# Kernel optimization log

Measured on AMD Instinct MI355X. Metric: run time of the kernel, lower is better.

Reference implementation:

```python
import jax, jax.numpy as jnp
import numpy as np

EPS = 1e-06
NUM_HEADS = 16


def _rms_norm(x, g, eps=EPS):
    # normalize over the last (full model) dim, as WanRMSNorm(dim)
    var = jnp.mean(jnp.square(x), axis=-1, keepdims=True)
    return x * jax.lax.rsqrt(var + eps) * g


def _apply_rope(q, k, freqs):
    # q, k: [b, s, n, d]; freqs: [s, d//2] angles. Interleaved (complex) pairs
    b, s, n, d = q.shape
    cos = jnp.cos(freqs)[None, :, None, :]  # [1, s, 1, d//2]
    sin = jnp.sin(freqs)[None, :, None, :]

    def rot(t):
        tr = t.reshape(b, s, n, d // 2, 2)
        t0, t1 = tr[..., 0], tr[..., 1]
        o0 = t0 * cos - t1 * sin
        o1 = t0 * sin + t1 * cos
        return jnp.stack([o0, o1], axis=-1).reshape(b, s, n, d)

    return rot(q), rot(k)


def setup_inputs() -> dict:
    key = jax.random.key(0)
    ks = jax.random.split(key, 8)
    b, s, dim = 2, 2048, 2048
    hd = dim // NUM_HEADS
    x = jax.random.normal(ks[0], (b, s, dim), dtype=jnp.float32)
    seq_lens = jax.random.randint(ks[1], (b,), s // 2, s + 1, dtype=jnp.int32)
    grid_sizes = jax.random.randint(ks[2], (b, 3), 1, 16).astype(jnp.int64)
    freqs = jax.random.uniform(ks[3], (s, hd // 2), dtype=jnp.float32) * 6.283
    sc = 1.0 / np.sqrt(dim)
    Wq = jax.random.normal(ks[4], (dim, dim), dtype=jnp.float32) * sc
    Wk = jax.random.normal(ks[5], (dim, dim), dtype=jnp.float32) * sc
    Wv = jax.random.normal(ks[6], (dim, dim), dtype=jnp.float32) * sc
    Wo = jax.random.normal(ks[7], (dim, dim), dtype=jnp.float32) * sc
    bo = jnp.zeros((dim,), dtype=jnp.float32)
    gq = jnp.ones((dim,), dtype=jnp.float32)
    gk = jnp.ones((dim,), dtype=jnp.float32)
    return {"x": x, "seq_lens": seq_lens, "grid_sizes": grid_sizes, "freqs": freqs,
            "Wq": Wq, "Wk": Wk, "Wv": Wv, "Wo": Wo, "bo": bo, "gq": gq, "gk": gk}


def reference(x, seq_lens, grid_sizes, freqs, Wq, Wk, Wv, Wo, bo, gq, gk):
    b, s, dim = x.shape
    n = NUM_HEADS
    d = dim // n
    scale = d ** (-0.5)

    # QKV projections (Linear: x @ W.T), with RMSNorm over full dim on q/k
    q = _rms_norm(x @ Wq.T, gq).reshape(b, s, n, d)
    k = _rms_norm(x @ Wk.T, gk).reshape(b, s, n, d)
    v = (x @ Wv.T).reshape(b, s, n, d)

    q, k = _apply_rope(q, k, freqs)

    # varlen attention: keys beyond seq_lens[b] are masked out
    scores = jnp.einsum("bqnd,bknd->bnqk", q, k) * scale
    key_valid = jnp.arange(s)[None, None, None, :] < seq_lens[:, None, None, None]
    scores = jnp.where(key_valid, scores, jnp.float32(-1e9))
    probs = jax.nn.softmax(scores, axis=-1)
    attn = jnp.einsum("bnqk,bknd->bqnd", probs, v).reshape(b, s, dim)

    return attn @ Wo.T + bo
```

## Files before the change

### kernel.cpp

```cpp
#include <hip/hip_runtime.h>
#include <hip/hip_bf16.h>
#include <math.h>

#define BATCH 2
#define SEQ   2048
#define DIM   2048
#define NH    16
#define HD    128
#define NROWS (BATCH * SEQ)
#define EPS_RMS 1e-6f

typedef unsigned short ushort_t;
typedef unsigned int   uint_t;
typedef __bf16    bf16x8 __attribute__((ext_vector_type(8)));
typedef _Float16  f16x8  __attribute__((ext_vector_type(8)));
typedef float     f32x4  __attribute__((ext_vector_type(4)));

__device__ inline ushort_t f2bf(float f) {
    uint_t u = __builtin_bit_cast(uint_t, f);
    uint_t r = u + 0x7FFFu + ((u >> 16) & 1u);
    return (ushort_t)(r >> 16);
}
__device__ inline ushort_t f2h(float f) {
    return __builtin_bit_cast(ushort_t, (_Float16)f);
}

__global__ __launch_bounds__(256) void cvt_all_kernel(
    const float* __restrict__ x,  const float* __restrict__ wq,
    const float* __restrict__ wk, const float* __restrict__ wv,
    const float* __restrict__ wo,
    ushort_t* __restrict__ xh,  ushort_t* __restrict__ wqh,
    ushort_t* __restrict__ wkh, ushort_t* __restrict__ wvh,
    ushort_t* __restrict__ woh)
{
    const int blk = blockIdx.x;
    const float* src; ushort_t* dst; size_t base;
    if (blk < 4096) { src = x; dst = xh; base = (size_t)blk * 2048; }
    else {
        const int r = blk - 4096;
        const int wsel = r >> 11;
        base = (size_t)(r & 2047) * 2048;
        if      (wsel == 0) { src = wq; dst = wqh; }
        else if (wsel == 1) { src = wk; dst = wkh; }
        else if (wsel == 2) { src = wv; dst = wvh; }
        else                { src = wo; dst = woh; }
    }
    const size_t i = base + ((size_t)threadIdx.x << 3);
    float v[8];
    *(float4*)&v[0] = *(const float4*)&src[i];
    *(float4*)&v[4] = *(const float4*)&src[i + 4];
    uint_t pk[4];
#pragma unroll
    for (int j = 0; j < 4; ++j)
        pk[j] = (uint_t)f2h(v[2 * j]) | ((uint_t)f2h(v[2 * j + 1]) << 16);
    *(uint4*)&dst[i] = make_uint4(pk[0], pk[1], pk[2], pk[3]);
}

template<int MODE>
__global__ __launch_bounds__(256, 2) void gemm_f16_kernel(
    const ushort_t* __restrict__ Ah, const ushort_t* __restrict__ Bh,
    const float* __restrict__ bias,
    float* __restrict__ C, ushort_t* __restrict__ Ct,
    const int M, const int N, const int K)
{
    __shared__ __align__(16) ushort_t sA[4096], sB[4096];
    const int tid  = threadIdx.x;
    const int w    = tid >> 6;
    const int lane = tid & 63;
    const int m0 = blockIdx.y * 128;
    const int n0 = blockIdx.x * 128;

    const int scol = (lane & 3) << 3;
    const int wr = w >> 1, wc = w & 1;
    const int fr = lane & 15, quad = lane >> 4;

    f32x4 acc[4][4];
#pragma unroll
    for (int mi = 0; mi < 4; ++mi)
#pragma unroll
        for (int ni = 0; ni < 4; ++ni)
            acc[mi][ni] = (f32x4){0.f, 0.f, 0.f, 0.f};

    for (int k0 = 0; k0 < K; k0 += 32) {
        __syncthreads();
#pragma unroll
        for (int it = 0; it < 2; ++it) {
            const int row  = (w << 5) + (it << 4) + (lane >> 2);
            const int loff = (w << 10) + (it << 9);
            const size_t ga = (size_t)(m0 + row) * K + k0 + scol;
            const size_t gb = (size_t)(n0 + row) * K + k0 + scol;
            __builtin_amdgcn_global_load_lds(
                (const __attribute__((address_space(1))) uint_t*)(const void*)(Ah + ga),
                (__attribute__((address_space(3))) uint_t*)(void*)&sA[loff], 16, 0, 0);
            __builtin_amdgcn_global_load_lds(
                (const __attribute__((address_space(1))) uint_t*)(const void*)(Bh + gb),
                (__attribute__((address_space(3))) uint_t*)(void*)&sB[loff], 16, 0, 0);
        }
        __syncthreads();

        f16x8 bfr[4];
#pragma unroll
        for (int ni = 0; ni < 4; ++ni) {
            const int row = (wc << 6) + (ni << 4) + fr;
            bfr[ni] = *(const f16x8*)&sB[(row << 5) + (quad << 3)];
        }
#pragma unroll
        for (int mi = 0; mi < 4; ++mi) {
            const int row = (wr << 6) + (mi << 4) + fr;
            const f16x8 ah = *(const f16x8*)&sA[(row << 5) + (quad << 3)];
#pragma unroll
            for (int ni = 0; ni < 4; ++ni)
                acc[mi][ni] = __builtin_amdgcn_mfma_f32_16x16x32_f16(ah, bfr[ni], acc[mi][ni], 0, 0, 0);
        }
    }

#pragma unroll
    for (int mi = 0; mi < 4; ++mi)
#pragma unroll
        for (int ni = 0; ni < 4; ++ni) {
            const int col = n0 + (wc << 6) + (ni << 4) + fr;
            if (MODE == 0) {
                const float bv = bias ? bias[col] : 0.f;
#pragma unroll
                for (int r = 0; r < 4; ++r) {
                    const int rowg = m0 + (wr << 6) + (mi << 4) + (quad << 2) + r;
                    C[(size_t)rowg * N + col] = acc[mi][ni][r] + bv;
                }
            } else {
                const int rowg = m0 + (wr << 6) + (mi << 4) + (quad << 2);
                const int bb = rowg >> 11, tok = rowg & (SEQ - 1);
                const int hh = col >> 7, d = col & (HD - 1);
                uint2 pk;
                pk.x = (uint_t)f2bf(acc[mi][ni][0]) | ((uint_t)f2bf(acc[mi][ni][1]) << 16);
                pk.y = (uint_t)f2bf(acc[mi][ni][2]) | ((uint_t)f2bf(acc[mi][ni][3]) << 16);
                *(uint2*)&Ct[((size_t)(bb * NH + hh) * HD + d) * SEQ + tok] = pk;
            }
        }
}

__global__ __launch_bounds__(256, 3) void qkv_gemm_kernel(
    const ushort_t* __restrict__ Ah, const ushort_t* __restrict__ Bq,
    const ushort_t* __restrict__ Bk, const ushort_t* __restrict__ Bv,
    float* __restrict__ Qb, float* __restrict__ Kb, ushort_t* __restrict__ Vt)
{
    __shared__ __align__(16) ushort_t sA[4096], sB[4096];
    const int tid  = threadIdx.x;
    const int w    = tid >> 6;
    const int lane = tid & 63;

    const int bid = blockIdx.x;
    const int nid = (bid & 7) * 192 + (bid >> 3);
    const int n_blk = nid >> 5;
    const int m_blk = nid & 31;
    const int wsel  = n_blk >> 4;
    const int m0 = m_blk * 128;
    const int n0 = (n_blk & 15) * 128;
    const ushort_t* __restrict__ Bh = (wsel == 0) ? Bq : (wsel == 1) ? Bk : Bv;

    const int scol = (lane & 3) << 3;
    const int wr = w >> 1, wc = w & 1;
    const int fr = lane & 15, quad = lane >> 4;

    f32x4 acc[4][4];
#pragma unroll
    for (int mi = 0; mi < 4; ++mi)
#pragma unroll
        for (int ni = 0; ni < 4; ++ni)
            acc[mi][ni] = (f32x4){0.f, 0.f, 0.f, 0.f};

    for (int k0 = 0; k0 < DIM; k0 += 32) {
        __syncthreads();
#pragma unroll
        for (int it = 0; it < 2; ++it) {
            const int row  = (w << 5) + (it << 4) + (lane >> 2);
            const int loff = (w << 10) + (it << 9);
            const size_t ga = (size_t)(m0 + row) * DIM + k0 + scol;
            const size_t gb = (size_t)(n0 + row) * DIM + k0 + scol;
            __builtin_amdgcn_global_load_lds(
                (const __attribute__((address_space(1))) uint_t*)(const void*)(Ah + ga),
                (__attribute__((address_space(3))) uint_t*)(void*)&sA[loff], 16, 0, 0);
            __builtin_amdgcn_global_load_lds(
                (const __attribute__((address_space(1))) uint_t*)(const void*)(Bh + gb),
                (__attribute__((address_space(3))) uint_t*)(void*)&sB[loff], 16, 0, 0);
        }
        __syncthreads();

        f16x8 bfr[4];
#pragma unroll
        for (int ni = 0; ni < 4; ++ni) {
            const int row = (wc << 6) + (ni << 4) + fr;
            bfr[ni] = *(const f16x8*)&sB[(row << 5) + (quad << 3)];
        }
#pragma unroll
        for (int mi = 0; mi < 4; ++mi) {
            const int row = (wr << 6) + (mi << 4) + fr;
            const f16x8 ah = *(const f16x8*)&sA[(row << 5) + (quad << 3)];
#pragma unroll
            for (int ni = 0; ni < 4; ++ni)
                acc[mi][ni] = __builtin_amdgcn_mfma_f32_16x16x32_f16(ah, bfr[ni], acc[mi][ni], 0, 0, 0);
        }
    }

    if (wsel < 2) {
        float* __restrict__ C = (wsel == 0) ? Qb : Kb;
#pragma unroll
        for (int mi = 0; mi < 4; ++mi)
#pragma unroll
            for (int ni = 0; ni < 4; ++ni) {
                const int col = n0 + (wc << 6) + (ni << 4) + fr;
#pragma unroll
                for (int r = 0; r < 4; ++r) {
                    const int rowg = m0 + (wr << 6) + (mi << 4) + (quad << 2) + r;
                    C[(size_t)rowg * DIM + col] = acc[mi][ni][r];
                }
            }
    } else {
#pragma unroll
        for (int mi = 0; mi < 4; ++mi)
#pragma unroll
            for (int ni = 0; ni < 4; ++ni) {
                const int col = n0 + (wc << 6) + (ni << 4) + fr;
                const int rowg = m0 + (wr << 6) + (mi << 4) + (quad << 2);
                const int bb = rowg >> 11, tok = rowg & (SEQ - 1);
                const int hh = col >> 7, d = col & (HD - 1);
                uint2 pk;
                pk.x = (uint_t)f2bf(acc[mi][ni][0]) | ((uint_t)f2bf(acc[mi][ni][1]) << 16);
                pk.y = (uint_t)f2bf(acc[mi][ni][2]) | ((uint_t)f2bf(acc[mi][ni][3]) << 16);
                *(uint2*)&Vt[((size_t)(bb * NH + hh) * HD + d) * SEQ + tok] = pk;
            }
    }
}

#define BM 64
#define BN 64
#define BK 16

__global__ __launch_bounds__(256) void gemm_nt_kernel(
    const float* __restrict__ A, const float* __restrict__ W,
    const float* __restrict__ bias, float* __restrict__ C,
    const int M, const int N, const int K)
{
    __shared__ float As[BK][BM + 4];
    __shared__ float Bs[BK][BN + 4];
    const int tid = threadIdx.x;
    const int tx = tid & 15;
    const int ty = tid >> 4;
    const int m0 = blockIdx.y * BM;
    const int n0 = blockIdx.x * BN;
    const int ldr = tid >> 2;
    const int ldc = (tid & 3) << 2;

    float acc[4][4] = {};

    for (int k0 = 0; k0 < K; k0 += BK) {
        __syncthreads();
        const float4 av = *(const float4*)&A[(size_t)(m0 + ldr) * K + (k0 + ldc)];
        const float4 wv = *(const float4*)&W[(size_t)(n0 + ldr) * K + (k0 + ldc)];
        As[ldc + 0][ldr] = av.x; As[ldc + 1][ldr] = av.y;
        As[ldc + 2][ldr] = av.z; As[ldc + 3][ldr] = av.w;
        Bs[ldc + 0][ldr] = wv.x; Bs[ldc + 1][ldr] = wv.y;
        Bs[ldc + 2][ldr] = wv.z; Bs[ldc + 3][ldr] = wv.w;
        __syncthreads();
#pragma unroll
        for (int k = 0; k < BK; ++k) {
            const float4 a4 = *(const float4*)&As[k][ty << 2];
            const float4 b4 = *(const float4*)&Bs[k][tx << 2];
            const float aa[4] = {a4.x, a4.y, a4.z, a4.w};
            const float bb[4] = {b4.x, b4.y, b4.z, b4.w};
#pragma unroll
            for (int i = 0; i < 4; ++i)
#pragma unroll
                for (int j = 0; j < 4; ++j)
                    acc[i][j] = fmaf(aa[i], bb[j], acc[i][j]);
        }
    }

#pragma unroll
    for (int i = 0; i < 4; ++i) {
        const int row = m0 + (ty << 2) + i;
        const int col = n0 + (tx << 2);
        float4 ov;
        ov.x = acc[i][0]; ov.y = acc[i][1]; ov.z = acc[i][2]; ov.w = acc[i][3];
        if (bias != nullptr) {
            ov.x += bias[col + 0]; ov.y += bias[col + 1];
            ov.z += bias[col + 2]; ov.w += bias[col + 3];
        }
        *(float4*)&C[(size_t)row * N + col] = ov;
    }
}

__global__ __launch_bounds__(256) void rmsnorm_rope_qk_kernel(
    const float* __restrict__ Qb, const float* __restrict__ gq,
    ushort_t* __restrict__ qbh,
    const float* __restrict__ Kb, const float* __restrict__ gk,
    ushort_t* __restrict__ kbh,
    const float* __restrict__ freqs)
{
    const int r = blockIdx.x;
    const int s = r & (SEQ - 1);
    const int tid = threadIdx.x;
    const int base = tid << 3;
    const bool isQ = (blockIdx.y == 0);
    const float* T = isQ ? Qb : Kb;
    const float* g = isQ ? gq : gk;
    ushort_t* out  = isQ ? qbh : kbh;
    const float posc = isQ ? 0.088388347648318447f : 1.0f;

    float v[8];
    *(float4*)&v[0] = *(const float4*)&T[(size_t)r * DIM + base];
    *(float4*)&v[4] = *(const float4*)&T[(size_t)r * DIM + base + 4];

    float ss = 0.f;
#pragma unroll
    for (int i = 0; i < 8; ++i) ss += v[i] * v[i];
#pragma unroll
    for (int off = 32; off > 0; off >>= 1) ss += __shfl_down(ss, off);

    __shared__ float wsum[4];
    __shared__ float inv_sh;
    if ((tid & 63) == 0) wsum[tid >> 6] = ss;
    __syncthreads();
    if (tid == 0)
        inv_sh = rsqrtf((wsum[0] + wsum[1] + wsum[2] + wsum[3]) * (1.0f / DIM) + EPS_RMS);
    __syncthreads();
    const float inv = inv_sh * posc;

    float gg[8];
    *(float4*)&gg[0] = *(const float4*)&g[base];
    *(float4*)&gg[4] = *(const float4*)&g[base + 4];
#pragma unroll
    for (int i = 0; i < 8; ++i) v[i] *= inv * gg[i];

    const int p0 = (base & (HD - 1)) >> 1;
#pragma unroll
    for (int pp = 0; pp < 4; ++pp) {
        float sn, cs;
        __sincosf(freqs[(size_t)s * (HD / 2) + p0 + pp], &sn, &cs);
        const float t0 = v[2 * pp], t1 = v[2 * pp + 1];
        v[2 * pp]     = t0 * cs - t1 * sn;
        v[2 * pp + 1] = t0 * sn + t1 * cs;
    }

    uint_t pk[4];
#pragma unroll
    for (int j = 0; j < 4; ++j)
        pk[j] = (uint_t)f2bf(v[2 * j]) | ((uint_t)f2bf(v[2 * j + 1]) << 16);
    *(uint4*)&out[(size_t)r * DIM + base] = make_uint4(pk[0], pk[1], pk[2], pk[3]);
}

__global__ __launch_bounds__(256) void rmsnorm_rope_kernel(
    float* __restrict__ T, const float* __restrict__ g,
    const float* __restrict__ freqs)
{
    const int r = blockIdx.x;
    const int s = r & (SEQ - 1);
    const int tid = threadIdx.x;
    const int base = tid << 3;

    float v[8];
    *(float4*)&v[0] = *(const float4*)&T[(size_t)r * DIM + base];
    *(float4*)&v[4] = *(const float4*)&T[(size_t)r * DIM + base + 4];

    float ss = 0.f;
#pragma unroll
    for (int i = 0; i < 8; ++i) ss += v[i] * v[i];
#pragma unroll
    for (int off = 32; off > 0; off >>= 1) ss += __shfl_down(ss, off);

    __shared__ float wsum[4];
    __shared__ float inv_sh;
    if ((tid & 63) == 0) wsum[tid >> 6] = ss;
    __syncthreads();
    if (tid == 0)
        inv_sh = rsqrtf((wsum[0] + wsum[1] + wsum[2] + wsum[3]) * (1.0f / DIM) + EPS_RMS);
    __syncthreads();
    const float inv = inv_sh;

    float gg[8];
    *(float4*)&gg[0] = *(const float4*)&g[base];
    *(float4*)&gg[4] = *(const float4*)&g[base + 4];
#pragma unroll
    for (int i = 0; i < 8; ++i) v[i] *= inv * gg[i];

    const int p0 = (base & (HD - 1)) >> 1;
#pragma unroll
    for (int pp = 0; pp < 4; ++pp) {
        float sn, cs;
        __sincosf(freqs[(size_t)s * (HD / 2) + p0 + pp], &sn, &cs);
        const float t0 = v[2 * pp], t1 = v[2 * pp + 1];
        v[2 * pp]     = t0 * cs - t1 * sn;
        v[2 * pp + 1] = t0 * sn + t1 * cs;
    }

    *(float4*)&T[(size_t)r * DIM + base]     = *(float4*)&v[0];
    *(float4*)&T[(size_t)r * DIM + base + 4] = *(float4*)&v[4];
}

#define AQ 128
#define AK 64
#define KSTR 136
#define VSTR 72
#define RESCALE_THR 8.0f

__global__ __launch_bounds__(256, 2) void attn_mfma_kernel(
    const ushort_t* __restrict__ QH, const ushort_t* __restrict__ KH,
    const ushort_t* __restrict__ VtG, const int* __restrict__ seq_lens,
    ushort_t* __restrict__ Oh)
{
    __shared__ __align__(16) ushort_t sK[AK * KSTR];
    __shared__ __align__(16) ushort_t sVt[HD * VSTR];
    __shared__ __align__(16) ushort_t sP[AQ * VSTR];

    const int tid  = threadIdx.x;
    const int w    = tid >> 6;
    const int lane = tid & 63;
    const int fr   = lane & 15;
    const int quad = lane >> 4;

    const int bid = blockIdx.x;
    const int sw  = (bid & 7) * 64 + (bid >> 3);
    const int q0  = (sw & 15) * AQ;
    const int hb  = sw >> 4;
    const int h   = hb & 15;
    const int b   = hb >> 4;
    const int len = seq_lens[b];

    bf16x8 qfrag[2][4];
#pragma unroll
    for (int qt = 0; qt < 2; ++qt)
#pragma unroll
        for (int h4 = 0; h4 < 4; ++h4) {
            const size_t qrow = (size_t)(b * SEQ + q0 + (w << 5) + (qt << 4) + fr);
            qfrag[qt][h4] = *(const bf16x8*)&QH[qrow * DIM + h * HD + (h4 << 5) + (quad << 3)];
        }

    f32x4 Oacc[2][8];
#pragma unroll
    for (int qt = 0; qt < 2; ++qt)
#pragma unroll
        for (int dt = 0; dt < 8; ++dt)
            Oacc[qt][dt] = (f32x4){0.f, 0.f, 0.f, 0.f};
    float mrow[2] = {-1.0e30f, -1.0e30f};
    float lrow[2] = {0.f, 0.f};

    const int ntiles = (len + AK - 1) / AK;
    for (int t = 0; t < ntiles; ++t) {
        const int k0 = t * AK;
        const bool masked = (k0 + AK > len);
        __syncthreads();
        for (int i = tid; i < AK * 16; i += 256) {
            const int key = i >> 4, c8 = (i & 15) << 3;
            const uint4 kv = *(const uint4*)&KH[(size_t)(b * SEQ + k0 + key) * DIM + h * HD + c8];
            *(uint4*)&sK[key * KSTR + c8] = kv;
        }
        for (int i = tid; i < HD * 8; i += 256) {
            const int d = i >> 3, kc = (i & 7) << 3;
            const uint4 vv = *(const uint4*)&VtG[((size_t)(b * NH + h) * HD + d) * SEQ + k0 + kc];
            *(uint4*)&sVt[d * VSTR + kc] = vv;
        }
        __syncthreads();

        f32x4 S[4][2];
        __builtin_amdgcn_s_setprio(1);
#pragma unroll
        for (int kt = 0; kt < 4; ++kt) {
            bf16x8 kf[4];
#pragma unroll
            for (int h4 = 0; h4 < 4; ++h4)
                kf[h4] = *(const bf16x8*)&sK[((kt << 4) + fr) * KSTR + (h4 << 5) + (quad << 3)];
#pragma unroll
            for (int qt = 0; qt < 2; ++qt) {
                f32x4 a = (f32x4){0.f, 0.f, 0.f, 0.f};
#pragma unroll
                for (int h4 = 0; h4 < 4; ++h4)
                    a = __builtin_amdgcn_mfma_f32_16x16x32_bf16(kf[h4], qfrag[qt][h4], a, 0, 0, 0);
                S[kt][qt] = a;
            }
        }
        __builtin_amdgcn_s_setprio(0);

#pragma unroll
        for (int qt = 0; qt < 2; ++qt) {
            float tm = -1.0e30f;
            if (masked) {
#pragma unroll
                for (int kt = 0; kt < 4; ++kt)
#pragma unroll
                    for (int r = 0; r < 4; ++r) {
                        const int key = k0 + (kt << 4) + (quad << 2) + r;
                        float s = (key < len) ? S[kt][qt][r] : -1.0e30f;
                        S[kt][qt][r] = s;
                        tm = fmaxf(tm, s);
                    }
            } else {
#pragma unroll
                for (int kt = 0; kt < 4; ++kt)
#pragma unroll
                    for (int r = 0; r < 4; ++r)
                        tm = fmaxf(tm, S[kt][qt][r]);
            }
            tm = fmaxf(tm, __shfl_xor(tm, 16));
            tm = fmaxf(tm, __shfl_xor(tm, 32));

            float mnew;
            if (__all(tm - mrow[qt] <= RESCALE_THR)) {
                mnew = mrow[qt];
            } else {
                mnew = fmaxf(mrow[qt], tm);
                const float alpha = __expf(mrow[qt] - mnew);
                mrow[qt] = mnew;
                lrow[qt] *= alpha;
#pragma unroll
                for (int r = 0; r < 4; ++r) {
                    const float ar = __shfl(alpha, (quad << 2) + r);
#pragma unroll
                    for (int dt = 0; dt < 8; ++dt)
                        Oacc[qt][dt][r] *= ar;
                }
            }

            float rsum = 0.f;
#pragma unroll
            for (int kt = 0; kt < 4; ++kt) {
                float p[4];
#pragma unroll
                for (int r = 0; r < 4; ++r) {
                    p[r] = __expf(S[kt][qt][r] - mnew);
                    rsum += p[r];
                }
                uint2 pk;
                pk.x = (uint_t)f2bf(p[0]) | ((uint_t)f2bf(p[1]) << 16);
                pk.y = (uint_t)f2bf(p[2]) | ((uint_t)f2bf(p[3]) << 16);
                *(uint2*)&sP[((w << 5) + (qt << 4) + fr) * VSTR + (kt << 4) + (quad << 2)] = pk;
            }
            rsum += __shfl_xor(rsum, 16);
            rsum += __shfl_xor(rsum, 32);
            lrow[qt] += rsum;
        }

        __builtin_amdgcn_s_setprio(1);
#pragma unroll
        for (int ks = 0; ks < 2; ++ks) {
            bf16x8 pf[2];
#pragma unroll
            for (int qt = 0; qt < 2; ++qt)
                pf[qt] = *(const bf16x8*)&sP[((w << 5) + (qt << 4) + fr) * VSTR + (ks << 5) + (quad << 3)];
#pragma unroll
            for (int dt = 0; dt < 8; ++dt) {
                const bf16x8 vf = *(const bf16x8*)&sVt[((dt << 4) + fr) * VSTR + (ks << 5) + (quad << 3)];
#pragma unroll
                for (int qt = 0; qt < 2; ++qt)
                    Oacc[qt][dt] = __builtin_amdgcn_mfma_f32_16x16x32_bf16(pf[qt], vf, Oacc[qt][dt], 0, 0, 0);
            }
        }
        __builtin_amdgcn_s_setprio(0);
    }

#pragma unroll
    for (int qt = 0; qt < 2; ++qt) {
        float linv[4];
#pragma unroll
        for (int r = 0; r < 4; ++r)
            linv[r] = 1.0f / __shfl(lrow[qt], (quad << 2) + r);
#pragma unroll
        for (int dt = 0; dt < 8; ++dt)
#pragma unroll
            for (int r = 0; r < 4; ++r) {
                const int qrow = q0 + (w << 5) + (qt << 4) + (quad << 2) + r;
                Oh[(size_t)(b * SEQ + qrow) * DIM + h * HD + (dt << 4) + fr] =
                    f2h(Oacc[qt][dt][r] * linv[r]);
            }
    }
}

#define BQ  64
#define BKT 64

__global__ __launch_bounds__(256) void attn_kernel(
    const float* __restrict__ Q, const float* __restrict__ K,
    const float* __restrict__ V, const int* __restrict__ seq_lens,
    float* __restrict__ O)
{
    const int qt = blockIdx.x;
    const int h  = blockIdx.y;
    const int b  = blockIdx.z;
    const int len = seq_lens[b];
    const int q0 = qt * BQ;
    const float scale = 0.088388347648318447f;

    __shared__ float Qst[HD][BQ + 4];
    __shared__ float Kst[HD][BKT + 4];
    __shared__ float Vs[BKT][HD + 4];
    __shared__ float Sc[BQ][BKT + 1];
    __shared__ float mrow[BQ], lrow[BQ], alpha_s[BQ];

    const int tid = threadIdx.x;
    const int si0 = (tid >> 4) << 2;
    const int sj0 = (tid & 15) << 2;
    const int pi0 = (tid >> 4) << 2;
    const int pc0 = (tid & 15) << 3;

    for (int i = tid; i < BQ * HD / 4; i += 256) {
        const int e = i << 2;
        const int row = e >> 7;
        const int c0 = e & (HD - 1);
        const float4 qv = *(const float4*)&Q[(size_t)(b * SEQ + q0 + row) * DIM + h * HD + c0];
        Qst[c0 + 0][row] = qv.x; Qst[c0 + 1][row] = qv.y;
        Qst[c0 + 2][row] = qv.z; Qst[c0 + 3][row] = qv.w;
    }
    if (tid < BQ) { mrow[tid] = -3.0e38f; lrow[tid] = 0.f; }

    float o[4][8] = {};
    __syncthreads();

    const int ntiles = (len + BKT - 1) / BKT;
    for (int t = 0; t < ntiles; ++t) {
        const int k0 = t * BKT;
        __syncthreads();
        for (int i = tid; i < BKT * HD / 4; i += 256) {
            const int e = i << 2;
            const int row = e >> 7;
            const int c0 = e & (HD - 1);
            const int kg = k0 + row;
            float4 kv = make_float4(0.f, 0.f, 0.f, 0.f);
            float4 vv = make_float4(0.f, 0.f, 0.f, 0.f);
            if (kg < len) {
                kv = *(const float4*)&K[(size_t)(b * SEQ + kg) * DIM + h * HD + c0];
                vv = *(const float4*)&V[(size_t)(b * SEQ + kg) * DIM + h * HD + c0];
            }
            Kst[c0 + 0][row] = kv.x; Kst[c0 + 1][row] = kv.y;
            Kst[c0 + 2][row] = kv.z; Kst[c0 + 3][row] = kv.w;
            *(float4*)&Vs[row][c0] = vv;
        }
        __syncthreads();

        float acc[4][4] = {};
#pragma unroll 8
        for (int kk = 0; kk < HD; ++kk) {
            const float4 q4 = *(const float4*)&Qst[kk][si0];
            const float4 k4 = *(const float4*)&Kst[kk][sj0];
            const float qa[4] = {q4.x, q4.y, q4.z, q4.w};
            const float ka[4] = {k4.x, k4.y, k4.z, k4.w};
#pragma unroll
            for (int i = 0; i < 4; ++i)
#pragma unroll
                for (int j = 0; j < 4; ++j)
                    acc[i][j] = fmaf(qa[i], ka[j], acc[i][j]);
        }
#pragma unroll
        for (int i = 0; i < 4; ++i)
#pragma unroll
            for (int j = 0; j < 4; ++j) {
                const int jg = k0 + sj0 + j;
                Sc[si0 + i][sj0 + j] = (jg < len) ? acc[i][j] * scale : -1.0e9f;
            }
        __syncthreads();

        if (tid < BQ) {
            const int i = tid;
            const float m_old = mrow[i];
            float mx = m_old;
            for (int j = 0; j < BKT; ++j) mx = fmaxf(mx, Sc[i][j]);
            const float al = __expf(m_old - mx);
            float sum = 0.f;
            for (int j = 0; j < BKT; ++j) {
                const float p = __expf(Sc[i][j] - mx);
                Sc[i][j] = p;
                sum += p;
            }
            mrow[i] = mx;
            lrow[i] = lrow[i] * al + sum;
            alpha_s[i] = al;
        }
        __syncthreads();

#pragma unroll
        for (int i = 0; i < 4; ++i) {
            const float al = alpha_s[pi0 + i];
#pragma unroll
            for (int c = 0; c < 8; ++c) o[i][c] *= al;
        }
        for (int j = 0; j < BKT; ++j) {
            float p[4];
#pragma unroll
            for (int i = 0; i < 4; ++i) p[i] = Sc[pi0 + i][j];
            const float4 v0 = *(const float4*)&Vs[j][pc0];
            const float4 v1 = *(const float4*)&Vs[j][pc0 + 4];
            const float va[8] = {v0.x, v0.y, v0.z, v0.w, v1.x, v1.y, v1.z, v1.w};
#pragma unroll
            for (int i = 0; i < 4; ++i)
#pragma unroll
                for (int c = 0; c < 8; ++c)
                    o[i][c] = fmaf(p[i], va[c], o[i][c]);
        }
    }

#pragma unroll
    for (int i = 0; i < 4; ++i) {
        const float invl = 1.0f / lrow[pi0 + i];
        float4 w0, w1;
        w0.x = o[i][0] * invl; w0.y = o[i][1] * invl;
        w0.z = o[i][2] * invl; w0.w = o[i][3] * invl;
        w1.x = o[i][4] * invl; w1.y = o[i][5] * invl;
        w1.z = o[i][6] * invl; w1.w = o[i][7] * invl;
        float* op = &O[(size_t)(b * SEQ + q0 + pi0 + i) * DIM + h * HD + pc0];
        *(float4*)&op[0] = w0;
        *(float4*)&op[4] = w1;
    }
}

extern "C" void kernel_launch(void* const* d_in, const int* in_sizes, int n_in,
                              void* d_out, int out_size, void* d_ws, size_t ws_size,
                              hipStream_t stream)
{
    const float* x        = (const float*)d_in[0];
    const int*   seq_lens = (const int*)d_in[1];
    const float* freqs    = (const float*)d_in[3];
    const float* Wq       = (const float*)d_in[4];
    const float* Wk       = (const float*)d_in[5];
    const float* Wv       = (const float*)d_in[6];
    const float* Wo       = (const float*)d_in[7];
    const float* bo       = (const float*)d_in[8];
    const float* gq       = (const float*)d_in[9];
    const float* gk       = (const float*)d_in[10];
    float* out = (float*)d_out;

    const size_t mat = (size_t)NROWS * DIM;
    const size_t wsz = (size_t)DIM * DIM;

    float*    Qb   = (float*)d_ws;
    float*    Kb   = Qb + mat;
    ushort_t* xh   = (ushort_t*)(Kb + mat);
    ushort_t* wqh  = xh + mat;
    ushort_t* wkh  = wqh + wsz;
    ushort_t* wvh  = wkh + wsz;
    ushort_t* woh  = wvh + wsz;
    ushort_t* qbh  = woh + wsz;
    ushort_t* kbh  = qbh + mat;
    ushort_t* vtg  = kbh + mat;
    ushort_t* abh  = vtg + mat;

    const size_t need = 2 * mat * sizeof(float)
                      + (mat + 4 * wsz + 4 * mat) * sizeof(ushort_t);

    if (ws_size >= need) {
        cvt_all_kernel<<<12288, 256, 0, stream>>>(
            x, Wq, Wk, Wv, Wo, xh, wqh, wkh, wvh, woh);

        qkv_gemm_kernel<<<1536, 256, 0, stream>>>(xh, wqh, wkh, wvh, Qb, Kb, vtg);

        rmsnorm_rope_qk_kernel<<<dim3(NROWS, 2), 256, 0, stream>>>(
            Qb, gq, qbh, Kb, gk, kbh, freqs);

        attn_mfma_kernel<<<512, 256, 0, stream>>>(qbh, kbh, vtg, seq_lens, abh);

        const dim3 gg(DIM / 128, NROWS / 128);
        gemm_f16_kernel<0><<<gg, 256, 0, stream>>>(abh, woh, bo, out, nullptr, NROWS, DIM, DIM);
    } else {
        float* Vb = Kb + mat;
        float* Ab = Vb + mat;
        const dim3 gemm_grid(DIM / BN, NROWS / BM);
        gemm_nt_kernel<<<gemm_grid, 256, 0, stream>>>(x, Wq, nullptr, Qb, NROWS, DIM, DIM);
        gemm_nt_kernel<<<gemm_grid, 256, 0, stream>>>(x, Wk, nullptr, Kb, NROWS, DIM, DIM);
        gemm_nt_kernel<<<gemm_grid, 256, 0, stream>>>(x, Wv, nullptr, Vb, NROWS, DIM, DIM);
        rmsnorm_rope_kernel<<<NROWS, 256, 0, stream>>>(Qb, gq, freqs);
        rmsnorm_rope_kernel<<<NROWS, 256, 0, stream>>>(Kb, gk, freqs);
        attn_kernel<<<dim3(SEQ / BQ, NH, BATCH), 256, 0, stream>>>(Qb, Kb, Vb, seq_lens, Ab);
        gemm_nt_kernel<<<gemm_grid, 256, 0, stream>>>(Ab, Wo, bo, out, NROWS, DIM, DIM);
    }
}
```

Baseline: 511.1 us.

## Raise occupancy, remap output GEMM blocks across XCDs, batch attention tile loads

Raises launch_bounds min blocks from 2 to 3 for the f16 GEMM and attention kernels so more waves can be resident per CU. Switches the output projection GEMM to a 1D grid whose block index is swizzled so each of the 8 XCDs gets a contiguous chunk of tiles, column-major over M, to improve L2 reuse of weight tiles. Unrolls the attention K/V tile copy into four independent global loads per thread issued before the LDS stores, to increase memory-level parallelism. The tighter register budget may cause spills in the MFMA-heavy kernels.

```diff
diff --git a/kernel.cpp b/kernel.cpp
--- a/kernel.cpp
+++ b/kernel.cpp
@@ -57,7 +57,7 @@
 }
 
 template<int MODE>
-__global__ __launch_bounds__(256, 2) void gemm_f16_kernel(
+__global__ __launch_bounds__(256, 3) void gemm_f16_kernel(
     const ushort_t* __restrict__ Ah, const ushort_t* __restrict__ Bh,
     const float* __restrict__ bias,
     float* __restrict__ C, ushort_t* __restrict__ Ct,
@@ -67,8 +67,15 @@
     const int tid  = threadIdx.x;
     const int w    = tid >> 6;
     const int lane = tid & 63;
-    const int m0 = blockIdx.y * 128;
-    const int n0 = blockIdx.x * 128;
+
+    const int bid   = blockIdx.x;
+    const int chunk = gridDim.x >> 3;
+    const int nid   = (bid & 7) * chunk + (bid >> 3);
+    const int mb    = M >> 7;
+    const int n_blk = nid / mb;
+    const int m_blk = nid - n_blk * mb;
+    const int m0 = m_blk * 128;
+    const int n0 = n_blk * 128;
 
     const int scol = (lane & 3) << 3;
     const int wr = w >> 1, wc = w & 1;
@@ -402,7 +409,7 @@
 #define VSTR 72
 #define RESCALE_THR 8.0f
 
-__global__ __launch_bounds__(256, 2) void attn_mfma_kernel(
+__global__ __launch_bounds__(256, 3) void attn_mfma_kernel(
     const ushort_t* __restrict__ QH, const ushort_t* __restrict__ KH,
     const ushort_t* __restrict__ VtG, const int* __restrict__ seq_lens,
     ushort_t* __restrict__ Oh)
@@ -443,20 +450,32 @@
     float mrow[2] = {-1.0e30f, -1.0e30f};
     float lrow[2] = {0.f, 0.f};
 
+    const int kr  = tid >> 4;
+    const int kc8 = (tid & 15) << 3;
+    const int vd  = tid >> 3;
+    const int vc8 = (tid & 7) << 3;
+    const size_t kbase = (size_t)(b * SEQ) * DIM + h * HD + kc8;
+    const size_t vbase = ((size_t)(b * NH + h) * HD) * SEQ + vc8;
+
     const int ntiles = (len + AK - 1) / AK;
     for (int t = 0; t < ntiles; ++t) {
         const int k0 = t * AK;
         const bool masked = (k0 + AK > len);
         __syncthreads();
-        for (int i = tid; i < AK * 16; i += 256) {
-            const int key = i >> 4, c8 = (i & 15) << 3;
-            const uint4 kv = *(const uint4*)&KH[(size_t)(b * SEQ + k0 + key) * DIM + h * HD + c8];
-            *(uint4*)&sK[key * KSTR + c8] = kv;
-        }
-        for (int i = tid; i < HD * 8; i += 256) {
-            const int d = i >> 3, kc = (i & 7) << 3;
-            const uint4 vv = *(const uint4*)&VtG[((size_t)(b * NH + h) * HD + d) * SEQ + k0 + kc];
-            *(uint4*)&sVt[d * VSTR + kc] = vv;
+        {
+            uint4 kv[4], vv[4];
+#pragma unroll
+            for (int j = 0; j < 4; ++j)
+                kv[j] = *(const uint4*)&KH[kbase + (size_t)(k0 + kr + (j << 4)) * DIM];
+#pragma unroll
+            for (int j = 0; j < 4; ++j)
+                vv[j] = *(const uint4*)&VtG[vbase + (size_t)(vd + (j << 5)) * SEQ + k0];
+#pragma unroll
+            for (int j = 0; j < 4; ++j)
+                *(uint4*)&sK[(kr + (j << 4)) * KSTR + kc8] = kv[j];
+#pragma unroll
+            for (int j = 0; j < 4; ++j)
+                *(uint4*)&sVt[(vd + (j << 5)) * VSTR + vc8] = vv[j];
         }
         __syncthreads();
 
@@ -754,8 +773,7 @@
 
         attn_mfma_kernel<<<512, 256, 0, stream>>>(qbh, kbh, vtg, seq_lens, abh);
 
-        const dim3 gg(DIM / 128, NROWS / 128);
-        gemm_f16_kernel<0><<<gg, 256, 0, stream>>>(abh, woh, bo, out, nullptr, NROWS, DIM, DIM);
+        gemm_f16_kernel<0><<<512, 256, 0, stream>>>(abh, woh, bo, out, nullptr, NROWS, DIM, DIM);
     } else {
         float* Vb = Kb + mat;
         float* Ab = Vb + mat;
```

Result: faster. 452.0 us (-11.6%).
